# Performance work log

Measured on AMD Instinct MI355X. Metric: run time of the kernel, lower is better.

## Reference

```python
import jax, jax.numpy as jnp
import numpy as np

B, S, HID = 1, 2048, 4096
H, KV, D, R = 32, 8, 128, 64   # heads, kv heads, head_dim, rotary_dim
EPS = 1e-6
THETA = 10000.0


def setup_inputs() -> dict:
    key = jax.random.key(0)
    ks = jax.random.split(key, 6)
    sc = 0.02
    return {
        'hidden_states': jax.random.normal(ks[0], (B, S, HID), jnp.float32),
        'Wq': jax.random.normal(ks[1], (H * D, HID), jnp.float32) * sc,
        'Wk': jax.random.normal(ks[2], (KV * D, HID), jnp.float32) * sc,
        'Wv': jax.random.normal(ks[3], (KV * D, HID), jnp.float32) * sc,
        'Wo': jax.random.normal(ks[4], (HID, H * D), jnp.float32) * sc,
        'q_norm_w': jnp.ones((H * D,), jnp.float32),
        'k_norm_w': jnp.ones((KV * D,), jnp.float32),
        'position_ids': jnp.broadcast_to(jnp.arange(S, dtype=jnp.int64)[None, :], (B, S)),
    }


def _rms_norm(x, w):
    xf = x.astype(jnp.float32)
    var = jnp.mean(xf * xf, axis=-1, keepdims=True)
    return (w * (xf * jax.lax.rsqrt(var + EPS))).astype(x.dtype)


def _rotate_half(x):
    x1, x2 = x[..., : R // 2], x[..., R // 2:]
    return jnp.concatenate((-x2, x1), axis=-1)


def reference(hidden_states, Wq, Wk, Wv, Wo, q_norm_w, k_norm_w, position_ids):
    x = hidden_states
    # projections (torch Linear: y = x @ W^T)
    q = jnp.einsum('bsd,od->bso', x, Wq)                      # [B,S,H*D]
    k = jnp.einsum('bsd,od->bso', x, Wk)                      # [B,S,KV*D]
    v = jnp.einsum('bsd,od->bso', x, Wv).reshape(B, S, KV, D)
    # QK RMSNorm over flattened head dims
    q = _rms_norm(q, q_norm_w).reshape(B, S, H, D)
    k = _rms_norm(k, k_norm_w).reshape(B, S, KV, D)
    # partial RoPE: rotary_dim=R out of head_dim=D
    inv_freq = 1.0 / (THETA ** (jnp.arange(0, R, 2, dtype=jnp.float32) / R))  # [R/2]
    freqs = position_ids.astype(jnp.float32)[..., None] * inv_freq            # [B,S,R/2]
    emb = jnp.concatenate((freqs, freqs), axis=-1)                            # [B,S,R]
    cos = jnp.cos(emb)[:, :, None, :]                                         # [B,S,1,R]
    sin = jnp.sin(emb)[:, :, None, :]
    q_rot = q[..., :R] * cos + _rotate_half(q[..., :R]) * sin
    k_rot = k[..., :R] * cos + _rotate_half(k[..., :R]) * sin
    q = jnp.concatenate((q_rot, q[..., R:]), axis=-1)
    k = jnp.concatenate((k_rot, k[..., R:]), axis=-1)
    # GQA repeat_kv
    G = H // KV
    k = jnp.repeat(k, G, axis=2)  # [B,S,H,D]
    v = jnp.repeat(v, G, axis=2)
    # attention with causal mask, softmax in fp32
    scaling = D ** -0.5
    scores = jnp.einsum('bqhd,bkhd->bhqk', q, k) * scaling    # [B,H,S,S]
    causal = jnp.tril(jnp.ones((S, S), dtype=bool))
    scores = jnp.where(causal[None, None], scores, jnp.finfo(jnp.float32).min)
    attn = jax.nn.softmax(scores.astype(jnp.float32), axis=-1).astype(q.dtype)
    out = jnp.einsum('bhqk,bkhd->bqhd', attn, v).reshape(B, S, H * D)
    return jnp.einsum('bso,do->bsd', out, Wo)
```

## Files before the change

kernel.cpp:

```cpp
#include <hip/hip_runtime.h>
#include <hip/hip_bf16.h>
#include <math.h>

typedef __bf16 bf16;
typedef __bf16 bf16x8 __attribute__((ext_vector_type(8)));
typedef float f32x4 __attribute__((ext_vector_type(4)));

#define S_LEN 2048
#define HID_D 4096
#define NH 32
#define NKV 8
#define HD 128
#define SCALE_LOG2 (0.08838834764831843f * 1.4426950408889634f)

__device__ __forceinline__ void gload_lds16(const void* g, void* lds) {
  __builtin_amdgcn_global_load_lds((__attribute__((address_space(1))) void*)g,
                                   (__attribute__((address_space(3))) void*)lds, 16, 0, 0);
}

#define MEMFENCE asm volatile("" ::: "memory")

__global__ __launch_bounds__(256) void cvt_kernel(const float* __restrict__ in,
                                                  bf16* __restrict__ out, int n8) {
  int i = blockIdx.x * blockDim.x + threadIdx.x;
  int stride = gridDim.x * blockDim.x;
  for (; i < n8; i += stride) {
    const float4* p = (const float4*)in + 2 * (size_t)i;
    float4 a = p[0], b = p[1];
    bf16x8 o;
    o[0] = (bf16)a.x; o[1] = (bf16)a.y; o[2] = (bf16)a.z; o[3] = (bf16)a.w;
    o[4] = (bf16)b.x; o[5] = (bf16)b.y; o[6] = (bf16)b.z; o[7] = (bf16)b.w;
    *((bf16x8*)out + i) = o;
  }
}

__global__ __launch_bounds__(256) void add_kernel(float* __restrict__ out,
                                                  const float* __restrict__ part, int n4) {
  int i = blockIdx.x * blockDim.x + threadIdx.x;
  int stride = gridDim.x * blockDim.x;
  for (; i < n4; i += stride) {
    float4 a = ((const float4*)out)[i];
    float4 b = ((const float4*)part)[i];
    a.x += b.x; a.y += b.y; a.z += b.z; a.w += b.w;
    ((float4*)out)[i] = a;
  }
}

__global__ __launch_bounds__(512, 2) void gemm256(const bf16* __restrict__ A,
                                                  const bf16* __restrict__ B,
                                                  float* __restrict__ C0,
                                                  float* __restrict__ C1,
                                                  int N, int Kfull, int Kslice, int T) {
  __shared__ __align__(16) char lds[131072];
  const int t = threadIdx.x, l = t & 63, w = t >> 6;
  const int wr = w >> 2, wc = w & 3;
  const int l15 = l & 15, lg = l >> 4;
  const int s7 = l15 & 7;

  const int nwg = gridDim.x * gridDim.y;
  const int lin = blockIdx.y * gridDim.x + blockIdx.x;
  const int swz = (lin & 7) * (nwg >> 3) + (lin >> 3);
  const int n0 = (swz % gridDim.x) * 256;
  const int m0 = (swz / gridDim.x) * 256;
  const size_t kbase = (size_t)blockIdx.z * Kslice;
  float* __restrict__ C = blockIdx.z ? C1 : C0;

  auto stage = [&](int d, int op, int hf, int tau) {
    char* dst = lds + d * 65536 + op * 32768 + hf * 16384;
    const bf16* src = op ? B : A;
    const int rbase = (op ? n0 : m0) + hf * 128;
    const size_t kpos = kbase + (size_t)tau * 64;
#pragma unroll
    for (int i = 0; i < 2; i++) {
      int q = i * 512 + t;
      int r = q >> 3;
      int c = (q & 7) ^ (r & 7);
      gload_lds16(src + (size_t)(rbase + r) * Kfull + kpos + c * 8, dst + q * 16);
    }
  };

  f32x4 acc[2][2][4][2] = {};
  bf16x8 a[4][2], b0[2][2], b1[2][2];

  auto ldsA = [&](int d, int hf) {
    const char* base = lds + d * 65536 + hf * 16384;
#pragma unroll
    for (int mf = 0; mf < 4; mf++) {
      int row = wr * 64 + mf * 16 + l15;
#pragma unroll
      for (int ks = 0; ks < 2; ks++)
        a[mf][ks] = *(const bf16x8*)(base + row * 128 + (((ks * 4 + lg) ^ s7) << 4));
    }
  };
  auto ldsB = [&](int d, int hf, bf16x8 bb[2][2]) {
    const char* base = lds + d * 65536 + 32768 + hf * 16384;
#pragma unroll
    for (int nf = 0; nf < 2; nf++) {
      int row = wc * 32 + nf * 16 + l15;
#pragma unroll
      for (int ks = 0; ks < 2; ks++)
        bb[nf][ks] = *(const bf16x8*)(base + row * 128 + (((ks * 4 + lg) ^ s7) << 4));
    }
  };

#define LEAD_BAR                                           \
  MEMFENCE; __builtin_amdgcn_s_barrier(); MEMFENCE;        \
  asm volatile("s_waitcnt lgkmcnt(0)" ::: "memory");       \
  __builtin_amdgcn_sched_barrier(0);
#define TRAIL_BAR MEMFENCE; __builtin_amdgcn_s_barrier(); MEMFENCE;

#define MMAQ(q, r, bb)                                                          \
  __builtin_amdgcn_s_setprio(1);                                               \
  _Pragma("unroll") for (int mf = 0; mf < 4; mf++)                              \
  _Pragma("unroll") for (int nf = 0; nf < 2; nf++)                              \
  _Pragma("unroll") for (int ks = 0; ks < 2; ks++)                              \
      acc[q][r][mf][nf] = __builtin_amdgcn_mfma_f32_16x16x32_bf16(              \
          a[mf][ks], bb[nf][ks], acc[q][r][mf][nf], 0, 0, 0);                   \
  __builtin_amdgcn_s_setprio(0);

  stage(0, 0, 0, 0); stage(0, 1, 0, 0); stage(0, 1, 1, 0); stage(0, 0, 1, 0);
  stage(1, 0, 0, 1); stage(1, 1, 0, 1); stage(1, 1, 1, 1);
  asm volatile("s_waitcnt vmcnt(6)" ::: "memory");
  TRAIL_BAR;

  for (int tau = 0; tau < T; tau++) {
    const int d = tau & 1, dn = d ^ 1;
    const bool s1 = tau + 1 < T, s2 = tau + 2 < T;
    if (s1) stage(dn, 0, 1, tau + 1);
    ldsA(d, 0); ldsB(d, 0, b0);
    LEAD_BAR; MMAQ(0, 0, b0); TRAIL_BAR;
    if (s2) stage(d, 0, 0, tau + 2);
    ldsB(d, 1, b1);
    LEAD_BAR; MMAQ(0, 1, b1); TRAIL_BAR;
    if (s2) stage(d, 1, 0, tau + 2);
    ldsA(d, 1);
    LEAD_BAR; MMAQ(1, 0, b0); TRAIL_BAR;
    if (s2) stage(d, 1, 1, tau + 2);
    if (s2) { asm volatile("s_waitcnt vmcnt(6)" ::: "memory"); }
    else    { asm volatile("s_waitcnt vmcnt(0)" ::: "memory"); }
    MEMFENCE; __builtin_amdgcn_s_barrier(); MEMFENCE;
    MMAQ(1, 1, b1); TRAIL_BAR;
  }

#pragma unroll
  for (int q = 0; q < 2; q++)
#pragma unroll
    for (int r = 0; r < 2; r++)
#pragma unroll
      for (int mf = 0; mf < 4; mf++) {
        int row = m0 + q * 128 + wr * 64 + mf * 16 + lg * 4;
#pragma unroll
        for (int nf = 0; nf < 2; nf++) {
          int col = n0 + r * 128 + wc * 32 + nf * 16 + l15;
          float* Cp = C + (size_t)row * N + col;
#pragma unroll
          for (int rr = 0; rr < 4; rr++) Cp[(size_t)rr * N] = acc[q][r][mf][nf][rr];
        }
      }
}

__global__ __launch_bounds__(256) void prep_kernel(const float* __restrict__ QKV,
                                                   const float* __restrict__ qw,
                                                   const float* __restrict__ kw,
                                                   const int* __restrict__ pos_ids,
                                                   bf16* __restrict__ Qb,
                                                   bf16* __restrict__ Kb,
                                                   bf16* __restrict__ Vt) {
  __shared__ __align__(16) float row[6144];
  __shared__ float cs[64];
  __shared__ float red[8];
  const int s = blockIdx.x, t = threadIdx.x;

  const float4* src = (const float4*)(QKV + (size_t)s * 6144);
#pragma unroll
  for (int i = 0; i < 6; i++) ((float4*)row)[t + i * 256] = src[t + i * 256];

  if (t < 32) {
    float p = (float)pos_ids[s];
    float ang = p * powf(10000.0f, -(float)t * (1.0f / 32.0f));
    float sn, cn;
    sincosf(ang, &sn, &cn);
    cs[t] = cn;
    cs[32 + t] = sn;
  }
  __syncthreads();

  float aq = 0.f, ak = 0.f;
  for (int i = t; i < 4096; i += 256) { float v = row[i]; aq += v * v; }
  for (int i = 4096 + t; i < 5120; i += 256) { float v = row[i]; ak += v * v; }
#pragma unroll
  for (int off = 32; off; off >>= 1) {
    aq += __shfl_down(aq, off);
    ak += __shfl_down(ak, off);
  }
  if ((t & 63) == 0) { red[t >> 6] = aq; red[4 + (t >> 6)] = ak; }
  __syncthreads();
  const float scq = rsqrtf((red[0] + red[1] + red[2] + red[3]) * (1.0f / 4096.0f) + 1e-6f);
  const float sck = rsqrtf((red[4] + red[5] + red[6] + red[7]) * (1.0f / 1024.0f) + 1e-6f);

  for (int e = t; e < 4096; e += 256) {
    int d = e & 127;
    int hh = e >> 7;
    float val = row[e] * scq * qw[e];
    float o;
    if (d < 32)       o = val * cs[d] - (row[e + 32] * scq * qw[e + 32]) * cs[32 + d];
    else if (d < 64)  o = val * cs[d - 32] + (row[e - 32] * scq * qw[e - 32]) * cs[d];
    else              o = val;
    Qb[((size_t)hh * S_LEN + s) * HD + d] = (bf16)o;
  }
  for (int e = t; e < 1024; e += 256) {
    int d = e & 127;
    int hh = e >> 7;
    int ri = 4096 + e;
    float val = row[ri] * sck * kw[e];
    float o;
    if (d < 32)       o = val * cs[d] - (row[ri + 32] * sck * kw[e + 32]) * cs[32 + d];
    else if (d < 64)  o = val * cs[d - 32] + (row[ri - 32] * sck * kw[e - 32]) * cs[d];
    else              o = val;
    Kb[((size_t)hh * S_LEN + s) * HD + d] = (bf16)o;
  }
  for (int e = t; e < 1024; e += 256) {
    int d = e & 127;
    int hh = e >> 7;
    Vt[((size_t)hh * HD + d) * S_LEN + s] = (bf16)row[5120 + e];
  }
}

__global__ __launch_bounds__(256, 2) void attn_kernel(const bf16* __restrict__ Qb,
                                                      const bf16* __restrict__ Kb,
                                                      const bf16* __restrict__ Vt,
                                                      bf16* __restrict__ Ctx) {
  __shared__ __align__(16) char KB[2][16384];
  __shared__ __align__(16) char VB[16384];
  __shared__ __align__(16) char PB[8192];
  const int t = threadIdx.x, l = t & 63, w = t >> 6;
  const int l15 = l & 15, lg = l >> 4;
  const int pairc = blockIdx.x >> 5;
  const int h = blockIdx.x & 31;

  const bf16* Kh = Kb + (size_t)(h >> 2) * S_LEN * HD;
  const bf16* Vh = Vt + (size_t)(h >> 2) * HD * S_LEN;
  char* Pw = PB + w * 2048;

  const int kslot = t;
  const int kj0 = kslot & 15;
  const int vj0 = kslot & 7;

#pragma unroll
  for (int phase = 0; phase < 2; phase++) {
    const int chunk = (phase == 0) ? pairc : (31 - pairc);
    const int ktiles = chunk + 1;
    const int q0 = chunk * 64 + w * 16;

    const bf16* Qh = Qb + ((size_t)h * S_LEN + q0) * HD;
    bf16x8 qf[4];
#pragma unroll
    for (int kk = 0; kk < 4; kk++)
      qf[kk] = *(const bf16x8*)(Qh + (size_t)l15 * HD + kk * 32 + lg * 8);

#pragma unroll
    for (int i = 0; i < 4; i++) {
      int r = (i * 256 + kslot) >> 4;
      const bf16* src = Kh + (size_t)r * HD + (((kj0 ^ (r & 7))) << 3);
      gload_lds16(src, KB[0] + (i * 256 + w * 64) * 16);
    }

    f32x4 O[8] = {};
    float m[4], lsum[4];
#pragma unroll
    for (int r = 0; r < 4; r++) { m[r] = -1e30f; lsum[r] = 0.f; }

    for (int tt = 0; tt < ktiles; tt++) {
      const int cur = tt & 1;
      const int kv0 = tt * 64;
      const char* Kcur = KB[cur];
      const bool hasnext = (tt + 1 < ktiles);

      MEMFENCE;
      __builtin_amdgcn_s_barrier();
      MEMFENCE;

#pragma unroll
      for (int i = 0; i < 4; i++) {
        int r = (i * 256 + kslot) >> 3;
        const bf16* src = Vh + (size_t)r * S_LEN + kv0 + ((vj0 ^ (r & 7)) << 3);
        gload_lds16(src, VB + (i * 256 + w * 64) * 16);
      }
      if (hasnext) {
#pragma unroll
        for (int i = 0; i < 4; i++) {
          int r = (i * 256 + kslot) >> 4;
          const bf16* src = Kh + (size_t)(kv0 + 64 + r) * HD + ((kj0 ^ (r & 7)) << 3);
          gload_lds16(src, KB[cur ^ 1] + (i * 256 + w * 64) * 16);
        }
        asm volatile("s_waitcnt vmcnt(8)" ::: "memory");
      } else {
        asm volatile("s_waitcnt vmcnt(4)" ::: "memory");
      }
      MEMFENCE;
      __builtin_amdgcn_s_barrier();
      MEMFENCE;

      f32x4 sc[4];
#pragma unroll
      for (int g = 0; g < 4; g++) sc[g] = (f32x4){0.f, 0.f, 0.f, 0.f};
#pragma unroll
      for (int g = 0; g < 4; g++) {
        const int r = g * 16 + l15;
        const char* Krow = Kcur + r * 256;
        const int sw = (r & 7);
#pragma unroll
        for (int kk = 0; kk < 4; kk++) {
          bf16x8 kf = *(const bf16x8*)(Krow + (((kk * 4 + lg) ^ sw) << 4));
          sc[g] = __builtin_amdgcn_mfma_f32_16x16x32_bf16(qf[kk], kf, sc[g], 0, 0, 0);
        }
      }

      const bool needmask = (kv0 + 63 > q0);
      float sv[4][4];
#pragma unroll
      for (int g = 0; g < 4; g++)
#pragma unroll
        for (int r = 0; r < 4; r++) {
          float x = sc[g][r] * SCALE_LOG2;
          if (needmask) {
            int kv = kv0 + g * 16 + l15;
            int qr = q0 + lg * 4 + r;
            if (kv > qr) x = -1e30f;
          }
          sv[g][r] = x;
        }
      float al[4];
#pragma unroll
      for (int r = 0; r < 4; r++) {
        float x = fmaxf(fmaxf(sv[0][r], sv[1][r]), fmaxf(sv[2][r], sv[3][r]));
        x = fmaxf(x, __shfl_xor(x, 1));
        x = fmaxf(x, __shfl_xor(x, 2));
        x = fmaxf(x, __shfl_xor(x, 4));
        x = fmaxf(x, __shfl_xor(x, 8));
        float mn = fmaxf(m[r], x);
        al[r] = exp2f(m[r] - mn);
        m[r] = mn;
      }
#pragma unroll
      for (int g = 0; g < 4; g++)
#pragma unroll
        for (int r = 0; r < 4; r++) sv[g][r] = exp2f(sv[g][r] - m[r]);
#pragma unroll
      for (int r = 0; r < 4; r++) {
        float x = (sv[0][r] + sv[1][r]) + (sv[2][r] + sv[3][r]);
        x += __shfl_xor(x, 1);
        x += __shfl_xor(x, 2);
        x += __shfl_xor(x, 4);
        x += __shfl_xor(x, 8);
        lsum[r] = lsum[r] * al[r] + x;
      }
#pragma unroll
      for (int dt = 0; dt < 8; dt++)
#pragma unroll
        for (int r = 0; r < 4; r++) O[dt][r] *= al[r];

#pragma unroll
      for (int g = 0; g < 4; g++)
#pragma unroll
        for (int r = 0; r < 4; r++) {
          int prow = lg * 4 + r;
          int pbyte = prow * 128 + (((g * 16 + l15) * 2) ^ ((prow & 7) << 4));
          *(bf16*)(Pw + pbyte) = (bf16)sv[g][r];
        }
      asm volatile("s_waitcnt lgkmcnt(0)" ::: "memory");
      bf16x8 pa[2];
#pragma unroll
      for (int ks = 0; ks < 2; ks++)
        pa[ks] = *(const bf16x8*)(Pw + l15 * 128 + (((ks * 4 + lg) ^ (l15 & 7)) << 4));

      if (hasnext) asm volatile("s_waitcnt vmcnt(4)" ::: "memory");
      else         asm volatile("s_waitcnt vmcnt(0)" ::: "memory");
      MEMFENCE;
      __builtin_amdgcn_s_barrier();
      MEMFENCE;

#pragma unroll
      for (int ks = 0; ks < 2; ks++)
#pragma unroll
        for (int dt = 0; dt < 8; dt++) {
          const int r = dt * 16 + l15;
          bf16x8 vf = *(const bf16x8*)(VB + r * 128 + (((ks * 4 + lg) ^ (r & 7)) << 4));
          O[dt] = __builtin_amdgcn_mfma_f32_16x16x32_bf16(pa[ks], vf, O[dt], 0, 0, 0);
        }
    }

#pragma unroll
    for (int r = 0; r < 4; r++) {
      float inv = 1.0f / lsum[r];
      bf16* Cp = Ctx + (size_t)(q0 + lg * 4 + r) * HID_D + h * HD + l15;
#pragma unroll
      for (int dt = 0; dt < 8; dt++) Cp[dt * 16] = (bf16)(O[dt][r] * inv);
    }
  }
}

extern "C" void kernel_launch(void* const* d_in, const int* in_sizes, int n_in,
                              void* d_out, int out_size, void* d_ws, size_t ws_size,
                              hipStream_t stream) {
  const float* X  = (const float*)d_in[0];
  const float* Wq = (const float*)d_in[1];
  const float* Wk = (const float*)d_in[2];
  const float* Wv = (const float*)d_in[3];
  const float* Wo = (const float*)d_in[4];
  const float* qw = (const float*)d_in[5];
  const float* kw = (const float*)d_in[6];
  const int* pos  = (const int*)d_in[7];

  char* ws = (char*)d_ws;
  bf16* Xb    = (bf16*)ws;
  bf16* Wqkvb = (bf16*)(ws + (16ll << 20));
  bf16* Wob   = Wqkvb;
  float* QKV  = (float*)(ws + (64ll << 20));
  float* Part = (float*)(ws + (64ll << 20));
  bf16* Ctx   = (bf16*)(ws + (96ll << 20));
  bf16* Qb    = (bf16*)(ws + (112ll << 20));
  bf16* Kb    = (bf16*)(ws + (128ll << 20));
  bf16* Vt    = (bf16*)(ws + (132ll << 20));

  cvt_kernel<<<2048, 256, 0, stream>>>(X, Xb, S_LEN * HID_D / 8);
  cvt_kernel<<<2048, 256, 0, stream>>>(Wq, Wqkvb, 4096 * 4096 / 8);
  cvt_kernel<<<512, 256, 0, stream>>>(Wk, Wqkvb + 4096 * 4096, 1024 * 4096 / 8);
  cvt_kernel<<<512, 256, 0, stream>>>(Wv, Wqkvb + 5120 * 4096, 1024 * 4096 / 8);

  gemm256<<<dim3(24, 8, 1), 512, 0, stream>>>(Xb, Wqkvb, QKV, QKV,
                                              6144, HID_D, HID_D, 64);

  cvt_kernel<<<2048, 256, 0, stream>>>(Wo, Wob, 4096 * 4096 / 8);

  prep_kernel<<<S_LEN, 256, 0, stream>>>(QKV, qw, kw, pos, Qb, Kb, Vt);

  attn_kernel<<<dim3(512), 256, 0, stream>>>(Qb, Kb, Vt, Ctx);

  gemm256<<<dim3(16, 8, 2), 512, 0, stream>>>(Ctx, Wob, (float*)d_out, Part,
                                              HID_D, HID_D, 2048, 32);
  add_kernel<<<2048, 256, 0, stream>>>((float*)d_out, Part, S_LEN * HID_D / 4);
}
```

Baseline: 391.8 us.

## Add 256x192 QKV GEMM, tiled V transpose kernel, double-buffer V in attention

```diff
diff --git a/kernel.cpp b/kernel.cpp
--- a/kernel.cpp
+++ b/kernel.cpp
@@ -46,6 +46,109 @@
   }
 }
 
+#define LEAD_BAR                                           \
+  MEMFENCE; __builtin_amdgcn_s_barrier(); MEMFENCE;        \
+  asm volatile("s_waitcnt lgkmcnt(0)" ::: "memory");       \
+  __builtin_amdgcn_sched_barrier(0);
+#define TRAIL_BAR MEMFENCE; __builtin_amdgcn_s_barrier(); MEMFENCE;
+
+__global__ __launch_bounds__(512, 2) void gemm192(const bf16* __restrict__ A,
+                                                  const bf16* __restrict__ B,
+                                                  float* __restrict__ C,
+                                                  int N, int Kfull, int T) {
+  __shared__ __align__(16) char lds[114688];
+  const int t = threadIdx.x, l = t & 63, w = t >> 6;
+  const int wr = w >> 2, wc = w & 3;
+  const int l15 = l & 15, lg = l >> 4;
+
+  const int nwg = gridDim.x * gridDim.y;
+  const int lin = blockIdx.y * gridDim.x + blockIdx.x;
+  const int swz = (lin & 7) * (nwg >> 3) + (lin >> 3);
+  const int n0 = (swz % gridDim.x) * 192;
+  const int m0 = (swz / gridDim.x) * 256;
+
+  auto stageAll = [&](int d, int tau) {
+    const size_t kpos = (size_t)tau * 64;
+#pragma unroll
+    for (int hf = 0; hf < 2; hf++) {
+      char* dst = lds + d * 57344 + hf * 16384;
+#pragma unroll
+      for (int i = 0; i < 2; i++) {
+        int q = i * 512 + t;
+        int r = q >> 3, c = (q & 7) ^ (r & 7);
+        gload_lds16(A + (size_t)(m0 + hf * 128 + r) * Kfull + kpos + c * 8, dst + q * 16);
+      }
+    }
+    char* dstB = lds + d * 57344 + 32768;
+#pragma unroll
+    for (int i = 0; i < 3; i++) {
+      int q = i * 512 + t;
+      int r = q >> 3, c = (q & 7) ^ (r & 7);
+      gload_lds16(B + (size_t)(n0 + r) * Kfull + kpos + c * 8, dstB + q * 16);
+    }
+  };
+
+  f32x4 acc[8][3] = {};
+  bf16x8 a[4], b[2][3];
+
+  auto ldsA = [&](int d, int q, int ks) {
+    const char* base = lds + d * 57344 + wr * 16384;
+#pragma unroll
+    for (int i = 0; i < 4; i++) {
+      int row = (q * 4 + i) * 16 + l15;
+      a[i] = *(const bf16x8*)(base + row * 128 + (((ks * 4 + lg) ^ (row & 7)) << 4));
+    }
+  };
+  auto ldsB = [&](int d, int ks) {
+    const char* base = lds + d * 57344 + 32768;
+#pragma unroll
+    for (int nf = 0; nf < 3; nf++) {
+      int row = wc * 48 + nf * 16 + l15;
+      b[ks][nf] = *(const bf16x8*)(base + row * 128 + (((ks * 4 + lg) ^ (row & 7)) << 4));
+    }
+  };
+
+#define MMA12(q, ks)                                                            \
+  __builtin_amdgcn_s_setprio(1);                                                \
+  _Pragma("unroll") for (int mf = 0; mf < 4; mf++)                              \
+  _Pragma("unroll") for (int nf = 0; nf < 3; nf++)                              \
+      acc[(q)*4 + mf][nf] = __builtin_amdgcn_mfma_f32_16x16x32_bf16(            \
+          a[mf], b[ks][nf], acc[(q)*4 + mf][nf], 0, 0, 0);                      \
+  __builtin_amdgcn_s_setprio(0);
+
+  stageAll(0, 0);
+  asm volatile("s_waitcnt vmcnt(0)" ::: "memory");
+  TRAIL_BAR;
+
+  for (int tau = 0; tau < T; tau++) {
+    const int d = tau & 1, dn = d ^ 1;
+    const bool s1 = tau + 1 < T;
+    if (s1) stageAll(dn, tau + 1);
+    ldsA(d, 0, 0); ldsB(d, 0);
+    LEAD_BAR; MMA12(0, 0); TRAIL_BAR;
+    ldsA(d, 1, 0);
+    LEAD_BAR; MMA12(1, 0); TRAIL_BAR;
+    ldsA(d, 0, 1); ldsB(d, 1);
+    LEAD_BAR; MMA12(0, 1); TRAIL_BAR;
+    ldsA(d, 1, 1);
+    if (s1) { asm volatile("s_waitcnt vmcnt(0)" ::: "memory"); }
+    LEAD_BAR; MMA12(1, 1); TRAIL_BAR;
+  }
+
+#pragma unroll
+  for (int fi = 0; fi < 8; fi++) {
+    int row = m0 + wr * 128 + fi * 16 + lg * 4;
+#pragma unroll
+    for (int nf = 0; nf < 3; nf++) {
+      int col = n0 + wc * 48 + nf * 16 + l15;
+      float* Cp = C + (size_t)row * N + col;
+#pragma unroll
+      for (int rr = 0; rr < 4; rr++) Cp[(size_t)rr * N] = acc[fi][nf][rr];
+    }
+  }
+#undef MMA12
+}
+
 __global__ __launch_bounds__(512, 2) void gemm256(const bf16* __restrict__ A,
                                                   const bf16* __restrict__ B,
                                                   float* __restrict__ C0,
@@ -103,14 +206,8 @@
     }
   };
 
-#define LEAD_BAR                                           \
-  MEMFENCE; __builtin_amdgcn_s_barrier(); MEMFENCE;        \
-  asm volatile("s_waitcnt lgkmcnt(0)" ::: "memory");       \
-  __builtin_amdgcn_sched_barrier(0);
-#define TRAIL_BAR MEMFENCE; __builtin_amdgcn_s_barrier(); MEMFENCE;
-
 #define MMAQ(q, r, bb)                                                          \
-  __builtin_amdgcn_s_setprio(1);                                               \
+  __builtin_amdgcn_s_setprio(1);                                                \
   _Pragma("unroll") for (int mf = 0; mf < 4; mf++)                              \
   _Pragma("unroll") for (int nf = 0; nf < 2; nf++)                              \
   _Pragma("unroll") for (int ks = 0; ks < 2; ks++)                              \
@@ -157,6 +254,31 @@
           for (int rr = 0; rr < 4; rr++) Cp[(size_t)rr * N] = acc[q][r][mf][nf][rr];
         }
       }
+#undef MMAQ
+}
+
+__global__ __launch_bounds__(256) void vt_kernel(const float* __restrict__ QKV,
+                                                 bf16* __restrict__ Vt) {
+  __shared__ __align__(16) float tile[64][68];
+  const int s0 = blockIdx.x * 64, d0 = blockIdx.y * 64;
+  const int t = threadIdx.x;
+#pragma unroll
+  for (int i = 0; i < 4; i++) {
+    int row = i * 16 + (t >> 4);
+    int c4 = t & 15;
+    float4 v = *(const float4*)(QKV + (size_t)(s0 + row) * 6144 + 5120 + d0 + c4 * 4);
+    *(float4*)&tile[row][c4 * 4] = v;
+  }
+  __syncthreads();
+#pragma unroll
+  for (int i = 0; i < 2; i++) {
+    int slot = i * 256 + t;
+    int dr = slot >> 3, ch = slot & 7;
+    bf16x8 o;
+#pragma unroll
+    for (int j = 0; j < 8; j++) o[j] = (bf16)tile[ch * 8 + j][dr];
+    *(bf16x8*)(Vt + (size_t)(d0 + dr) * S_LEN + s0 + ch * 8) = o;
+  }
 }
 
 __global__ __launch_bounds__(256) void prep_kernel(const float* __restrict__ QKV,
@@ -164,16 +286,15 @@
                                                    const float* __restrict__ kw,
                                                    const int* __restrict__ pos_ids,
                                                    bf16* __restrict__ Qb,
-                                                   bf16* __restrict__ Kb,
-                                                   bf16* __restrict__ Vt) {
-  __shared__ __align__(16) float row[6144];
+                                                   bf16* __restrict__ Kb) {
+  __shared__ __align__(16) float row[5120];
   __shared__ float cs[64];
   __shared__ float red[8];
   const int s = blockIdx.x, t = threadIdx.x;
 
   const float4* src = (const float4*)(QKV + (size_t)s * 6144);
 #pragma unroll
-  for (int i = 0; i < 6; i++) ((float4*)row)[t + i * 256] = src[t + i * 256];
+  for (int i = 0; i < 5; i++) ((float4*)row)[t + i * 256] = src[t + i * 256];
 
   if (t < 32) {
     float p = (float)pos_ids[s];
@@ -219,11 +340,6 @@
     else              o = val;
     Kb[((size_t)hh * S_LEN + s) * HD + d] = (bf16)o;
   }
-  for (int e = t; e < 1024; e += 256) {
-    int d = e & 127;
-    int hh = e >> 7;
-    Vt[((size_t)hh * HD + d) * S_LEN + s] = (bf16)row[5120 + e];
-  }
 }
 
 __global__ __launch_bounds__(256, 2) void attn_kernel(const bf16* __restrict__ Qb,
@@ -231,7 +347,7 @@
                                                       const bf16* __restrict__ Vt,
                                                       bf16* __restrict__ Ctx) {
   __shared__ __align__(16) char KB[2][16384];
-  __shared__ __align__(16) char VB[16384];
+  __shared__ __align__(16) char VB[2][16384];
   __shared__ __align__(16) char PB[8192];
   const int t = threadIdx.x, l = t & 63, w = t >> 6;
   const int l15 = l & 15, lg = l >> 4;
@@ -242,9 +358,25 @@
   const bf16* Vh = Vt + (size_t)(h >> 2) * HD * S_LEN;
   char* Pw = PB + w * 2048;
 
-  const int kslot = t;
-  const int kj0 = kslot & 15;
-  const int vj0 = kslot & 7;
+  const int kj0 = t & 15;
+  const int vj0 = t & 7;
+
+  auto stageK = [&](int buf, int kvbase) {
+#pragma unroll
+    for (int i = 0; i < 4; i++) {
+      int r = (i * 256 + t) >> 4;
+      const bf16* src = Kh + (size_t)(kvbase + r) * HD + ((kj0 ^ (r & 7)) << 3);
+      gload_lds16(src, KB[buf] + (i * 256 + w * 64) * 16);
+    }
+  };
+  auto stageV = [&](int buf, int kvbase) {
+#pragma unroll
+    for (int i = 0; i < 4; i++) {
+      int r = (i * 256 + t) >> 3;
+      const bf16* src = Vh + (size_t)r * S_LEN + kvbase + ((vj0 ^ (r & 7)) << 3);
+      gload_lds16(src, VB[buf] + (i * 256 + w * 64) * 16);
+    }
+  };
 
 #pragma unroll
   for (int phase = 0; phase < 2; phase++) {
@@ -258,12 +390,8 @@
     for (int kk = 0; kk < 4; kk++)
       qf[kk] = *(const bf16x8*)(Qh + (size_t)l15 * HD + kk * 32 + lg * 8);
 
-#pragma unroll
-    for (int i = 0; i < 4; i++) {
-      int r = (i * 256 + kslot) >> 4;
-      const bf16* src = Kh + (size_t)r * HD + (((kj0 ^ (r & 7))) << 3);
-      gload_lds16(src, KB[0] + (i * 256 + w * 64) * 16);
-    }
+    stageK(0, 0);
+    stageV(0, 0);
 
     f32x4 O[8] = {};
     float m[4], lsum[4];
@@ -276,27 +404,7 @@
       const char* Kcur = KB[cur];
       const bool hasnext = (tt + 1 < ktiles);
 
-      MEMFENCE;
-      __builtin_amdgcn_s_barrier();
-      MEMFENCE;
-
-#pragma unroll
-      for (int i = 0; i < 4; i++) {
-        int r = (i * 256 + kslot) >> 3;
-        const bf16* src = Vh + (size_t)r * S_LEN + kv0 + ((vj0 ^ (r & 7)) << 3);
-        gload_lds16(src, VB + (i * 256 + w * 64) * 16);
-      }
-      if (hasnext) {
-#pragma unroll
-        for (int i = 0; i < 4; i++) {
-          int r = (i * 256 + kslot) >> 4;
-          const bf16* src = Kh + (size_t)(kv0 + 64 + r) * HD + ((kj0 ^ (r & 7)) << 3);
-          gload_lds16(src, KB[cur ^ 1] + (i * 256 + w * 64) * 16);
-        }
-        asm volatile("s_waitcnt vmcnt(8)" ::: "memory");
-      } else {
-        asm volatile("s_waitcnt vmcnt(4)" ::: "memory");
-      }
+      asm volatile("s_waitcnt vmcnt(0)" ::: "memory");
       MEMFENCE;
       __builtin_amdgcn_s_barrier();
       MEMFENCE;
@@ -314,6 +422,11 @@
           bf16x8 kf = *(const bf16x8*)(Krow + (((kk * 4 + lg) ^ sw) << 4));
           sc[g] = __builtin_amdgcn_mfma_f32_16x16x32_bf16(qf[kk], kf, sc[g], 0, 0, 0);
         }
+      }
+
+      if (hasnext) {
+        stageK(cur ^ 1, kv0 + 64);
+        stageV(cur ^ 1, kv0 + 64);
       }
 
       const bool needmask = (kv0 + 63 > q0);
@@ -374,21 +487,19 @@
       for (int ks = 0; ks < 2; ks++)
         pa[ks] = *(const bf16x8*)(Pw + l15 * 128 + (((ks * 4 + lg) ^ (l15 & 7)) << 4));
 
-      if (hasnext) asm volatile("s_waitcnt vmcnt(4)" ::: "memory");
-      else         asm volatile("s_waitcnt vmcnt(0)" ::: "memory");
-      MEMFENCE;
-      __builtin_amdgcn_s_barrier();
-      MEMFENCE;
-
 #pragma unroll
       for (int ks = 0; ks < 2; ks++)
 #pragma unroll
         for (int dt = 0; dt < 8; dt++) {
           const int r = dt * 16 + l15;
-          bf16x8 vf = *(const bf16x8*)(VB + r * 128 + (((ks * 4 + lg) ^ (r & 7)) << 4));
+          bf16x8 vf = *(const bf16x8*)(VB[cur] + r * 128 + (((ks * 4 + lg) ^ (r & 7)) << 4));
           O[dt] = __builtin_amdgcn_mfma_f32_16x16x32_bf16(pa[ks], vf, O[dt], 0, 0, 0);
         }
     }
+
+    MEMFENCE;
+    __builtin_amdgcn_s_barrier();
+    MEMFENCE;
 
 #pragma unroll
     for (int r = 0; r < 4; r++) {
@@ -428,12 +539,12 @@
   cvt_kernel<<<512, 256, 0, stream>>>(Wk, Wqkvb + 4096 * 4096, 1024 * 4096 / 8);
   cvt_kernel<<<512, 256, 0, stream>>>(Wv, Wqkvb + 5120 * 4096, 1024 * 4096 / 8);
 
-  gemm256<<<dim3(24, 8, 1), 512, 0, stream>>>(Xb, Wqkvb, QKV, QKV,
-                                              6144, HID_D, HID_D, 64);
+  gemm192<<<dim3(32, 8, 1), 512, 0, stream>>>(Xb, Wqkvb, QKV, 6144, HID_D, 64);
 
   cvt_kernel<<<2048, 256, 0, stream>>>(Wo, Wob, 4096 * 4096 / 8);
 
-  prep_kernel<<<S_LEN, 256, 0, stream>>>(QKV, qw, kw, pos, Qb, Kb, Vt);
+  vt_kernel<<<dim3(32, 16), 256, 0, stream>>>(QKV, Vt);
+  prep_kernel<<<S_LEN, 256, 0, stream>>>(QKV, qw, kw, pos, Qb, Kb);
 
   attn_kernel<<<dim3(512), 256, 0, stream>>>(Qb, Kb, Vt, Ctx);
 
```

Measured after the change: 379.2 us. -3.2%, faster.
